# Performance work log

Hardware: AMD Instinct MI355X
Metric: run time of the kernel (lower is better)

Reference implementation:

```python
import jax, jax.numpy as jnp
import numpy as np

GAMMA = 0.96875
SCALE_BASE = 512.0


def _fixed_pos_embedding(scale):
    # scale: (L, d) where d = head_dim // 2
    L, d = scale.shape
    inv_freq = 1.0 / (10000.0 ** (jnp.arange(d, dtype=jnp.float32) / d))
    sinusoid = jnp.arange(L, dtype=jnp.float32)[:, None] * inv_freq  # (L, d)
    return jnp.sin(sinusoid), jnp.cos(sinusoid)


def _rotate_every_two(x):
    # (..., D) -> (..., D) with pairs (x0, x1) -> (-x1, x0)
    x1 = x[..., ::2]
    x2 = x[..., 1::2]
    return jnp.stack((-x2, x1), axis=-1).reshape(x.shape)


def _dup_interleave(m):
    # (L, d) -> (L, 2d), each column duplicated (matches rotary pairing)
    return jnp.repeat(m, 2, axis=-1)


def xpos(x, offset=0, downscale=False):
    # x: (B, S, D). Standard torchscale-style XPos rotary embedding.
    S, D = x.shape[-2], x.shape[-1]
    scale_vec = (jnp.arange(0, D, 2, dtype=jnp.float32) + 0.4 * D) / (1.4 * D)  # (D/2,)
    min_pos = -(S + offset) // 2
    max_pos = S + offset + min_pos
    power = jnp.arange(min_pos, max_pos, dtype=jnp.float32) / SCALE_BASE  # (S+offset,)
    scale = scale_vec ** power[:, None]  # (S+offset, D/2)
    sin, cos = _fixed_pos_embedding(scale)
    if scale.shape[0] > S:  # keep the last S positions
        scale, sin, cos = scale[-S:], sin[-S:], cos[-S:]
    if downscale:
        scale = 1.0 / scale
    sin = _dup_interleave(sin * scale)  # (S, D)
    cos = _dup_interleave(cos * scale)  # (S, D)
    return x * cos + _rotate_every_two(x) * sin


def _decay_mask(S, dtype):
    # D[n, m] = gamma^(n-m) if n >= m else 0  (lower triangular)
    m = jnp.arange(S)
    diff = m[:, None] - m  # (S, S)
    causal = diff >= 0
    exp = jnp.where(causal, diff, 0).astype(dtype)
    return jnp.where(causal, jnp.asarray(GAMMA, dtype) ** exp, jnp.zeros((), dtype))


def setup_inputs() -> dict:
    key = jax.random.key(0)
    kx, kq, kk, kv = jax.random.split(key, 4)
    B, S, H, Dh = 4, 4096, 2048, 256
    return {
        "x": jax.random.normal(kx, (B, S, H), dtype=jnp.float32),
        "w_q": jax.random.normal(kq, (H, Dh), dtype=jnp.float32),
        "w_k": jax.random.normal(kk, (H, Dh), dtype=jnp.float32),
        "w_v": jax.random.normal(kv, (H, Dh), dtype=jnp.float32),
    }


def reference(x, w_q, w_k, w_v):
    # x: (B, S, H) -> out: (B, S, Dh)
    B, S, _ = x.shape
    decay = _decay_mask(S, x.dtype)[None]  # (1, S, S)
    q = xpos(x @ w_q)                       # (B, S, Dh)
    k = xpos(x @ w_k, downscale=True)       # (B, S, Dh)
    v = x @ w_v                             # (B, S, Dh)
    ret = jnp.einsum("bsd,btd->bst", q, k) * decay  # (B, S, S)
    return jnp.einsum("bst,btd->bsd", ret, v)       # (B, S, Dh)
```

## Files before the change

kernel.cpp:

```cpp
#include <hip/hip_runtime.h>
#include <cstddef>
#include <cstdint>

#define Bn 4
#define Sn 4096
#define Hn 2048
#define Dn 256

typedef float f32x16 __attribute__((ext_vector_type(16)));
typedef short bf16x8 __attribute__((ext_vector_type(8)));

#define AS3 __attribute__((address_space(3)))
#define AS1 __attribute__((address_space(1)))

#define L2G -0.045803689613125f
#define GC 2.9526131e-4f

__device__ __forceinline__ unsigned short f2bf(float f) {
  union { float f; unsigned int u; } a; a.f = f;
  unsigned int r = a.u + 0x7fffu + ((a.u >> 16) & 1u);
  return (unsigned short)(r >> 16);
}
__device__ __forceinline__ float bf2f(unsigned int b) {
  union { unsigned int u; float f; } a; a.u = b << 16;
  return a.f;
}

__global__ __launch_bounds__(256) void xbf_kernel(const float* __restrict__ x,
                                                  unsigned short* __restrict__ xb) {
  const size_t g = (size_t)blockIdx.x * 256 + threadIdx.x;
  const float* src = x + g * 16;
  unsigned short* dst = xb + g * 16;
  uint4 o0, o1;
  {
    float4 v0 = ((const float4*)src)[0];
    float4 v1 = ((const float4*)src)[1];
    float4 v2 = ((const float4*)src)[2];
    float4 v3 = ((const float4*)src)[3];
    o0.x = f2bf(v0.x) | ((unsigned int)f2bf(v0.y) << 16);
    o0.y = f2bf(v0.z) | ((unsigned int)f2bf(v0.w) << 16);
    o0.z = f2bf(v1.x) | ((unsigned int)f2bf(v1.y) << 16);
    o0.w = f2bf(v1.z) | ((unsigned int)f2bf(v1.w) << 16);
    o1.x = f2bf(v2.x) | ((unsigned int)f2bf(v2.y) << 16);
    o1.y = f2bf(v2.z) | ((unsigned int)f2bf(v2.w) << 16);
    o1.z = f2bf(v3.x) | ((unsigned int)f2bf(v3.y) << 16);
    o1.w = f2bf(v3.z) | ((unsigned int)f2bf(v3.w) << 16);
  }
  ((uint4*)dst)[0] = o0;
  ((uint4*)dst)[1] = o1;
}

__global__ __launch_bounds__(256) void wt_build(const float* __restrict__ wq,
                                                const float* __restrict__ wk,
                                                const float* __restrict__ wv,
                                                unsigned short* __restrict__ wt) {
  __shared__ __align__(16) unsigned short T[64][72];
  const int tid = threadIdx.x;
  const int k0 = blockIdx.x * 64;
  const int n0 = blockIdx.y * 64;
  const float* w = (n0 < 256) ? wq : (n0 < 512 ? wk : wv);
  const int nc0 = n0 & 255;
#pragma unroll
  for (int it = 0; it < 2; ++it) {
    int flat = it * 256 + tid;
    int r = flat >> 3, c8 = flat & 7;
    const float* src = w + (size_t)(k0 + r) * 256 + nc0 + c8 * 8;
    float4 v0 = *(const float4*)src;
    float4 v1 = *(const float4*)(src + 4);
    T[c8 * 8 + 0][r] = f2bf(v0.x); T[c8 * 8 + 1][r] = f2bf(v0.y);
    T[c8 * 8 + 2][r] = f2bf(v0.z); T[c8 * 8 + 3][r] = f2bf(v0.w);
    T[c8 * 8 + 4][r] = f2bf(v1.x); T[c8 * 8 + 5][r] = f2bf(v1.y);
    T[c8 * 8 + 6][r] = f2bf(v1.z); T[c8 * 8 + 7][r] = f2bf(v1.w);
  }
  __syncthreads();
#pragma unroll
  for (int it = 0; it < 2; ++it) {
    int flat = it * 256 + tid;
    int nr = flat >> 3, kc8 = flat & 7;
    int n = n0 + nr;
    int kc_sw = kc8 ^ (n & 7);
    uint4 val = *(const uint4*)&T[nr][kc8 * 8];
    *(uint4*)((char*)wt + (size_t)n * 4096 + (size_t)k0 * 2 + kc_sw * 16) = val;
  }
}

__global__ __launch_bounds__(256, 3) void proj2_kernel(const unsigned short* __restrict__ xb,
                                                       const unsigned short* __restrict__ wt,
                                                       unsigned short* __restrict__ qkv) {
  __shared__ __align__(16) unsigned short As[128 * 64];
  __shared__ __align__(16) unsigned short Bs[128 * 64];
  const int tid = threadIdx.x;
  const int lane = tid & 63;
  const int wid = tid >> 6;
  const int wr = wid >> 1, wc = wid & 1;
  const int m0 = blockIdx.x * 128;
  const int n0 = blockIdx.y * 128;
  const int l31 = lane & 31, lh = lane >> 5;

  f32x16 acc[2][2];
#pragma unroll
  for (int i = 0; i < 2; ++i)
#pragma unroll
    for (int j = 0; j < 2; ++j) acc[i][j] = 0.0f;

  for (int k0 = 0; k0 < Hn; k0 += 64) {
    AS3 char* ldsa = (AS3 char*)As;
    AS3 char* ldsb = (AS3 char*)Bs;
#pragma unroll
    for (int i = 0; i < 4; ++i) {
      int ou = i * 4096 + wid * 1024;
      int o = ou + lane * 16;
      int row = o >> 7, colB = o & 127;
      const char* srcA = (const char*)xb + (size_t)(m0 + row) * 4096 + k0 * 2 + (colB ^ ((row & 7) << 4));
      __builtin_amdgcn_global_load_lds((const AS1 unsigned int*)srcA,
                                       (AS3 unsigned int*)(ldsa + ou), 16, 0, 0);
      const char* srcB = (const char*)wt + (size_t)(n0 + row) * 4096 + k0 * 2 + colB;
      __builtin_amdgcn_global_load_lds((const AS1 unsigned int*)srcB,
                                       (AS3 unsigned int*)(ldsb + ou), 16, 0, 0);
    }
    __syncthreads();
#pragma unroll
    for (int kc = 0; kc < 4; ++kc) {
      const int kb = kc * 32 + lh * 16;
      bf16x8 a[2], b[2];
#pragma unroll
      for (int i = 0; i < 2; ++i) {
        int mr = wr * 64 + i * 32 + l31;
        a[i] = *(const bf16x8*)((const char*)As + mr * 128 + (kb ^ ((mr & 7) << 4)));
        int nr = wc * 64 + i * 32 + l31;
        b[i] = *(const bf16x8*)((const char*)Bs + nr * 128 + (kb ^ ((nr & 7) << 4)));
      }
#pragma unroll
      for (int i = 0; i < 2; ++i)
#pragma unroll
        for (int j = 0; j < 2; ++j)
          acc[i][j] = __builtin_amdgcn_mfma_f32_32x32x16_bf16(a[i], b[j], acc[i][j], 0, 0, 0);
    }
    __syncthreads();
  }
  const bool khalf = (n0 >= 256 && n0 < 512);
#pragma unroll
  for (int i = 0; i < 2; ++i)
#pragma unroll
    for (int j = 0; j < 2; ++j)
#pragma unroll
      for (int reg = 0; reg < 16; ++reg) {
        int m = m0 + wr * 64 + i * 32 + (reg & 3) + 8 * (reg >> 2) + 4 * lh;
        int n = n0 + wc * 64 + j * 32 + l31;
        if (khalf) n = 256 + ((n - 256) ^ ((m & 7) << 3));
        qkv[(size_t)m * 768 + n] = f2bf(acc[i][j][reg]);
      }
}

__global__ __launch_bounds__(256, 2) void proj_kernel(const float* __restrict__ x,
                                                      const unsigned short* __restrict__ wt,
                                                      unsigned short* __restrict__ qkv) {
  __shared__ __align__(16) unsigned short As[128 * 64];
  __shared__ __align__(16) unsigned short Bs[128 * 64];
  const int tid = threadIdx.x;
  const int lane = tid & 63;
  const int wid = tid >> 6;
  const int wr = wid >> 1, wc = wid & 1;
  const int m0 = blockIdx.x * 128;
  const int n0 = blockIdx.y * 128;
  const int l31 = lane & 31, lh = lane >> 5;

  f32x16 acc[2][2];
#pragma unroll
  for (int i = 0; i < 2; ++i)
#pragma unroll
    for (int j = 0; j < 2; ++j) acc[i][j] = 0.0f;

  for (int k0 = 0; k0 < Hn; k0 += 64) {
    {
      AS3 char* ldsb = (AS3 char*)Bs;
#pragma unroll
      for (int i = 0; i < 4; ++i) {
        int ou = i * 4096 + wid * 1024;
        int o = ou + lane * 16;
        int row = o >> 7, col = o & 127;
        const char* src = (const char*)wt + (size_t)(n0 + row) * 4096 + k0 * 2 + col;
        __builtin_amdgcn_global_load_lds((const AS1 unsigned int*)src,
                                         (AS3 unsigned int*)(ldsb + ou), 16, 0, 0);
      }
    }
#pragma unroll
    for (int i = 0; i < 4; ++i) {
      int o = i * 256 + tid;
      int row = o >> 3, c8 = o & 7;
      const float* src = x + (size_t)(m0 + row) * 2048 + k0 + c8 * 8;
      float4 v0 = *(const float4*)src;
      float4 v1 = *(const float4*)(src + 4);
      uint4 val;
      val.x = f2bf(v0.x) | ((unsigned int)f2bf(v0.y) << 16);
      val.y = f2bf(v0.z) | ((unsigned int)f2bf(v0.w) << 16);
      val.z = f2bf(v1.x) | ((unsigned int)f2bf(v1.y) << 16);
      val.w = f2bf(v1.z) | ((unsigned int)f2bf(v1.w) << 16);
      *(uint4*)((char*)As + row * 128 + ((c8 * 16) ^ ((row & 7) << 4))) = val;
    }
    __syncthreads();
#pragma unroll
    for (int kc = 0; kc < 4; ++kc) {
      const int kb = kc * 32 + lh * 16;
      bf16x8 a[2], b[2];
#pragma unroll
      for (int i = 0; i < 2; ++i) {
        int mr = wr * 64 + i * 32 + l31;
        a[i] = *(const bf16x8*)((const char*)As + mr * 128 + (kb ^ ((mr & 7) << 4)));
        int nr = wc * 64 + i * 32 + l31;
        b[i] = *(const bf16x8*)((const char*)Bs + nr * 128 + (kb ^ ((nr & 7) << 4)));
      }
#pragma unroll
      for (int i = 0; i < 2; ++i)
#pragma unroll
        for (int j = 0; j < 2; ++j)
          acc[i][j] = __builtin_amdgcn_mfma_f32_32x32x16_bf16(a[i], b[j], acc[i][j], 0, 0, 0);
    }
    __syncthreads();
  }
  const bool khalf = (n0 >= 256 && n0 < 512);
#pragma unroll
  for (int i = 0; i < 2; ++i)
#pragma unroll
    for (int j = 0; j < 2; ++j)
#pragma unroll
      for (int reg = 0; reg < 16; ++reg) {
        int m = m0 + wr * 64 + i * 32 + (reg & 3) + 8 * (reg >> 2) + 4 * lh;
        int n = n0 + wc * 64 + j * 32 + l31;
        if (khalf) n = 256 + ((n - 256) ^ ((m & 7) << 3));
        qkv[(size_t)m * 768 + n] = f2bf(acc[i][j][reg]);
      }
}

__global__ __launch_bounds__(256) void xpos_kernel(unsigned short* __restrict__ qkv) {
  const int g = blockIdx.x * 256 + threadIdx.x;
  const int m = g >> 5;
  const int c = g & 31;
  const float s = (float)(m & (Sn - 1));
  unsigned short* qrow = qkv + (size_t)m * 768;
  const int csw = c ^ (m & 7);
  uint4 qv = *(uint4*)(qrow + c * 8);
  uint4 kv = *(uint4*)(qrow + 256 + csw * 8);
  unsigned int* qu = (unsigned int*)&qv;
  unsigned int* ku = (unsigned int*)&kv;
  const float pw = (s - 2048.0f) * (1.0f / 512.0f);
  const float gp = exp2f((float)(m & 255) * L2G);
#pragma unroll
  for (int p = 0; p < 4; ++p) {
    const int jp = c * 4 + p;
    const float invf = exp2f((float)jp * (-13.287712379549449f / 128.0f));
    float sn, cs;
    sincosf(s * invf, &sn, &cs);
    const float sv = (2.0f * jp + 102.4f) * (1.0f / 358.4f);
    const float scq = exp2f(pw * log2f(sv)) * gp;
    const float sci = 1.0f / scq;
    float q0 = bf2f(qu[p] & 0xffffu), q1 = bf2f(qu[p] >> 16);
    float k0 = bf2f(ku[p] & 0xffffu), k1 = bf2f(ku[p] >> 16);
    float q0r = (q0 * cs - q1 * sn) * scq;
    float q1r = (q1 * cs + q0 * sn) * scq;
    float k0r = (k0 * cs - k1 * sn) * sci;
    float k1r = (k1 * cs + k0 * sn) * sci;
    qu[p] = f2bf(q0r) | ((unsigned int)f2bf(q1r) << 16);
    ku[p] = f2bf(k0r) | ((unsigned int)f2bf(k1r) << 16);
  }
  *(uint4*)(qrow + c * 8) = qv;
  *(uint4*)(qrow + 256 + csw * 8) = kv;
}

__global__ __launch_bounds__(256) void kvt_build(const unsigned short* __restrict__ qkv,
                                                 unsigned short* __restrict__ kt,
                                                 unsigned short* __restrict__ vt) {
  __shared__ __align__(16) unsigned short Tk[64][72];
  __shared__ __align__(16) unsigned short Tv[64][72];
  const int tid = threadIdx.x;
  const int t0 = blockIdx.x * 64;
  const int d0 = blockIdx.y * 64;
  const int b = blockIdx.z;
  const size_t rowb = ((size_t)b * Sn + t0) * 1536;
#pragma unroll
  for (int it = 0; it < 2; ++it) {
    int flat = it * 256 + tid;
    int r = flat >> 3, c8 = flat & 7;
    int kc = (d0 >> 3) + c8;
    int kcs = kc ^ (r & 7);
    uint4 kvv = *(const uint4*)((const char*)qkv + rowb + (size_t)r * 1536 + 512 + kcs * 16);
    uint4 vvv = *(const uint4*)((const char*)qkv + rowb + (size_t)r * 1536 + 1024 + (size_t)(d0 + c8 * 8) * 2);
    const unsigned short* ke = (const unsigned short*)&kvv;
    const unsigned short* ve = (const unsigned short*)&vvv;
#pragma unroll
    for (int e = 0; e < 8; ++e) { Tk[c8 * 8 + e][r] = ke[e]; Tv[c8 * 8 + e][r] = ve[e]; }
  }
  __syncthreads();
#pragma unroll
  for (int it = 0; it < 2; ++it) {
    int flat = it * 256 + tid;
    int dr = flat >> 3, tc8 = flat & 7;
    *(uint4*)(kt + (size_t)(b * 256 + d0 + dr) * 4096 + t0 + tc8 * 8) = *(const uint4*)&Tk[dr][tc8 * 8];
    *(uint4*)(vt + (size_t)(b * 256 + d0 + dr) * 4096 + t0 + tc8 * 8) = *(const uint4*)&Tv[dr][tc8 * 8];
  }
}

__global__ __launch_bounds__(256) void mbuild_kernel(const unsigned short* __restrict__ kt,
                                                     const unsigned short* __restrict__ vt,
                                                     unsigned short* __restrict__ mt) {
  const int tid = threadIdx.x;
  const int lane = tid & 63;
  const int wid = tid >> 6;
  const int l31 = lane & 31, lh = lane >> 5;
  const int jc = blockIdx.x;
  const int quad = blockIdx.y;
  const int b = blockIdx.z;
  const int d2w = ((quad >> 1) * 2 + (wid >> 1)) * 64;
  const int d1w = ((quad & 1) * 2 + (wid & 1)) * 64;
  const size_t tb = (size_t)jc * 256;

  f32x16 acc[2][2];
#pragma unroll
  for (int i = 0; i < 2; ++i)
#pragma unroll
    for (int j = 0; j < 2; ++j) acc[i][j] = 0.0f;

#pragma unroll 2
  for (int dc = 0; dc < 16; ++dc) {
    const int ko = dc * 32 + lh * 16;
    bf16x8 a[2], bb[2];
#pragma unroll
    for (int i = 0; i < 2; ++i) {
      a[i]  = *(const bf16x8*)((const char*)vt + ((size_t)(b * 256 + d2w + i * 32 + l31) * 4096 + tb) * 2 + ko);
      bb[i] = *(const bf16x8*)((const char*)kt + ((size_t)(b * 256 + d1w + i * 32 + l31) * 4096 + tb) * 2 + ko);
    }
#pragma unroll
    for (int i = 0; i < 2; ++i)
#pragma unroll
      for (int j = 0; j < 2; ++j)
        acc[i][j] = __builtin_amdgcn_mfma_f32_32x32x16_bf16(a[i], bb[j], acc[i][j], 0, 0, 0);
  }
  unsigned short* dst = mt + ((size_t)(b * 16 + jc) << 16);
#pragma unroll
  for (int i = 0; i < 2; ++i)
#pragma unroll
    for (int j = 0; j < 2; ++j)
#pragma unroll
      for (int reg = 0; reg < 16; ++reg) {
        int row = d2w + i * 32 + (reg & 3) + 8 * (reg >> 2) + 4 * lh;
        int col = d1w + j * 32 + l31;
        dst[row * 256 + col] = f2bf(acc[i][j][reg]);
      }
}

__global__ __launch_bounds__(256) void scan_kernel(unsigned short* __restrict__ mt) {
  const int e0 = (blockIdx.x * 256 + threadIdx.x) * 4;
  const int b = blockIdx.y;
  unsigned short* base = mt + ((size_t)b << 20);
  float s0 = 0.f, s1 = 0.f, s2 = 0.f, s3 = 0.f;
  for (int j = 1; j < 16; ++j) {
    unsigned short* p = base + ((size_t)(j - 1) << 16) + e0;
    uint2 mv = *(const uint2*)p;
    s0 = GC * (s0 + bf2f(mv.x & 0xffffu));
    s1 = GC * (s1 + bf2f(mv.x >> 16));
    s2 = GC * (s2 + bf2f(mv.y & 0xffffu));
    s3 = GC * (s3 + bf2f(mv.y >> 16));
    uint2 w;
    w.x = f2bf(s0) | ((unsigned int)f2bf(s1) << 16);
    w.y = f2bf(s2) | ((unsigned int)f2bf(s3) << 16);
    *(uint2*)p = w;
  }
}

__global__ __launch_bounds__(256, 2) void retc_kernel(const unsigned short* __restrict__ qkv,
                                                      const unsigned short* __restrict__ vt,
                                                      const unsigned short* __restrict__ mt,
                                                      float* __restrict__ out) {
  __shared__ float cmb[2][32][256];
  const int tid = threadIdx.x;
  const int lane = tid & 63;
  const int wid = tid >> 6;
  const int tw = wid & 1, sw = wid >> 1;
  const int l31 = lane & 31, lh = lane >> 5;
  const int st = blockIdx.x;
  const int b = blockIdx.y;
  const int j = st >> 2;
  const int s0w = st * 64 + sw * 32;

  bf16x8 qf[16];
  {
    const char* qrow = (const char*)qkv + ((size_t)b * Sn + s0w + l31) * 1536;
#pragma unroll
    for (int dc = 0; dc < 16; ++dc)
      qf[dc] = *(const bf16x8*)(qrow + dc * 32 + lh * 16);
  }

  f32x16 acc[8];
#pragma unroll
  for (int i = 0; i < 8; ++i) acc[i] = 0.0f;

  if (j > 0) {
    const char* Sj = (const char*)mt + ((size_t)(b * 16 + j - 1) << 17);
#pragma unroll 2
    for (int dc = 0; dc < 16; ++dc) {
#pragma unroll
      for (int g = 0; g < 4; ++g) {
        const int ng = tw * 4 + g;
        const int d2 = ng * 32 + l31;
        bf16x8 sbf = *(const bf16x8*)(Sj + d2 * 512 + dc * 32 + lh * 16);
        acc[ng] = __builtin_amdgcn_mfma_f32_32x32x16_bf16(qf[dc], sbf, acc[ng], 0, 0, 0);
      }
    }
  }

  const int sg = s0w + l31;
  const int ksw = (l31 & 7) << 4;
  for (int tt = (st & ~3); tt <= st; ++tt) {
    const bool diag = (tt == st);
    if (diag && tw > sw) break;
    const int t0 = tt * 64 + tw * 32;
    const bool msk = diag && (tw == sw);

    f32x16 sacc = 0.0f;
    const char* krow = (const char*)qkv + ((size_t)b * Sn + t0 + l31) * 1536 + 512;
#pragma unroll 4
    for (int dc = 0; dc < 16; ++dc) {
      bf16x8 kf = *(const bf16x8*)(krow + ((dc * 32 + lh * 16) ^ ksw));
      sacc = __builtin_amdgcn_mfma_f32_32x32x16_bf16(kf, qf[dc], sacc, 0, 0, 0);
    }
    unsigned int P[8];
#pragma unroll
    for (int k = 0; k < 8; ++k) {
      const int r0 = 2 * k;
      float f0 = sacc[r0], f1 = sacc[r0 + 1];
      if (msk) {
        const int tg0 = t0 + (r0 & 3) + 8 * (r0 >> 2) + 4 * lh;
        f0 = (sg - tg0 >= 0) ? f0 : 0.0f;
        f1 = (sg - tg0 - 1 >= 0) ? f1 : 0.0f;
      }
      unsigned int pk;
      asm("v_cvt_pk_bf16_f32 %0, %1, %2" : "=v"(pk) : "v"(f0), "v"(f1));
      P[k] = pk;
    }
    asm volatile("v_permlane32_swap_b32 %0, %1" : "+v"(P[0]), "+v"(P[2]));
    asm volatile("v_permlane32_swap_b32 %0, %1" : "+v"(P[1]), "+v"(P[3]));
    asm volatile("v_permlane32_swap_b32 %0, %1" : "+v"(P[4]), "+v"(P[6]));
    asm volatile("v_permlane32_swap_b32 %0, %1" : "+v"(P[5]), "+v"(P[7]));
#pragma unroll
    for (int kc = 0; kc < 2; ++kc) {
      uint4 pw;
      pw.x = P[kc * 4 + 0]; pw.y = P[kc * 4 + 1];
      pw.z = P[kc * 4 + 2]; pw.w = P[kc * 4 + 3];
      bf16x8 pf = *(const bf16x8*)&pw;
#pragma unroll
      for (int ng = 0; ng < 8; ++ng) {
        const int d = ng * 32 + l31;
        bf16x8 vf = *(const bf16x8*)((const char*)vt +
            ((size_t)(b * 256 + d) * 4096 + t0) * 2 + kc * 32 + lh * 16);
        acc[ng] = __builtin_amdgcn_mfma_f32_32x32x16_bf16(pf, vf, acc[ng], 0, 0, 0);
      }
    }
  }

  if (tw == 1) {
#pragma unroll
    for (int ng = 0; ng < 8; ++ng)
#pragma unroll
      for (int reg = 0; reg < 16; ++reg) {
        int sl = (reg & 3) + 8 * (reg >> 2) + 4 * lh;
        cmb[sw][sl][ng * 32 + l31] = acc[ng][reg];
      }
  }
  __syncthreads();
  if (tw == 0) {
#pragma unroll
    for (int ng = 0; ng < 8; ++ng)
#pragma unroll
      for (int reg = 0; reg < 16; ++reg) {
        int sl = (reg & 3) + 8 * (reg >> 2) + 4 * lh;
        int d = ng * 32 + l31;
        out[((size_t)(b * Sn + st * 64 + sw * 32 + sl)) * 256 + d] = acc[ng][reg] + cmb[sw][sl][d];
      }
  }
}

extern "C" void kernel_launch(void* const* d_in, const int* in_sizes, int n_in,
                              void* d_out, int out_size, void* d_ws, size_t ws_size,
                              hipStream_t stream) {
  (void)in_sizes; (void)n_in; (void)out_size;
  const float* x  = (const float*)d_in[0];
  const float* wq = (const float*)d_in[1];
  const float* wk = (const float*)d_in[2];
  const float* wv = (const float*)d_in[3];
  float* out = (float*)d_out;
  char* ws = (char*)d_ws;

  unsigned short* qkv = (unsigned short*)(ws);
  unsigned short* vt  = (unsigned short*)(ws + 25165824);
  unsigned short* kt  = (unsigned short*)(ws + 33554432);
  unsigned short* mt  = (unsigned short*)(ws + 41943040);

  const size_t NEED_BIG = 95420416;
  if (ws_size >= NEED_BIG) {
    unsigned short* xb = (unsigned short*)(ws + 25165824);
    unsigned short* wt = (unsigned short*)(ws + 92274688);
    xbf_kernel<<<8192, 256, 0, stream>>>(x, xb);
    wt_build<<<dim3(32, 12), 256, 0, stream>>>(wq, wk, wv, wt);
    proj2_kernel<<<dim3(128, 6), 256, 0, stream>>>(xb, wt, qkv);
  } else {
    unsigned short* wt = (unsigned short*)(ws + 41943040);
    wt_build<<<dim3(32, 12), 256, 0, stream>>>(wq, wk, wv, wt);
    proj_kernel<<<dim3(128, 6), 256, 0, stream>>>(x, wt, qkv);
  }
  xpos_kernel<<<2048, 256, 0, stream>>>(qkv);
  kvt_build<<<dim3(64, 4, 4), 256, 0, stream>>>(qkv, kt, vt);
  mbuild_kernel<<<dim3(16, 4, 4), 256, 0, stream>>>(kt, vt, mt);
  scan_kernel<<<dim3(64, 4), 256, 0, stream>>>(mt);
  retc_kernel<<<dim3(64, 4), 256, 0, stream>>>(qkv, vt, mt, out);
}
```

Before: 192.7 us.

## Split retention output kernel over head-dim halves and 32-row tiles

```diff
diff --git a/kernel.cpp b/kernel.cpp
--- a/kernel.cpp
+++ b/kernel.cpp
@@ -371,58 +371,62 @@
                                                       const unsigned short* __restrict__ vt,
                                                       const unsigned short* __restrict__ mt,
                                                       float* __restrict__ out) {
-  __shared__ float cmb[2][32][256];
+  __shared__ float cmb[2][32][128];
   const int tid = threadIdx.x;
   const int lane = tid & 63;
-  const int wid = tid >> 6;
-  const int tw = wid & 1, sw = wid >> 1;
+  const int tw = tid >> 6;
   const int l31 = lane & 31, lh = lane >> 5;
   const int st = blockIdx.x;
-  const int b = blockIdx.y;
-  const int j = st >> 2;
-  const int s0w = st * 64 + sw * 32;
+  const int dh = blockIdx.y;
+  const int b = blockIdx.z;
+  const int j = st >> 3;
+  const int base = st & ~7;
+  const int s0 = st * 32;
+  const int d0 = dh * 128;
 
   bf16x8 qf[16];
   {
-    const char* qrow = (const char*)qkv + ((size_t)b * Sn + s0w + l31) * 1536;
+    const char* qrow = (const char*)qkv + ((size_t)b * Sn + s0 + l31) * 1536;
 #pragma unroll
     for (int dc = 0; dc < 16; ++dc)
       qf[dc] = *(const bf16x8*)(qrow + dc * 32 + lh * 16);
   }
 
-  f32x16 acc[8];
-#pragma unroll
-  for (int i = 0; i < 8; ++i) acc[i] = 0.0f;
+  f32x16 acc[4];
+#pragma unroll
+  for (int i = 0; i < 4; ++i) acc[i] = 0.0f;
 
   if (j > 0) {
     const char* Sj = (const char*)mt + ((size_t)(b * 16 + j - 1) << 17);
-#pragma unroll 2
-    for (int dc = 0; dc < 16; ++dc) {
+#pragma unroll
+    for (int dcl = 0; dcl < 4; ++dcl) {
+      const int dc = tw * 4 + dcl;
 #pragma unroll
       for (int g = 0; g < 4; ++g) {
-        const int ng = tw * 4 + g;
-        const int d2 = ng * 32 + l31;
-        bf16x8 sbf = *(const bf16x8*)(Sj + d2 * 512 + dc * 32 + lh * 16);
-        acc[ng] = __builtin_amdgcn_mfma_f32_32x32x16_bf16(qf[dc], sbf, acc[ng], 0, 0, 0);
-      }
-    }
-  }
-
-  const int sg = s0w + l31;
+        const int d2 = d0 + g * 32 + l31;
+        bf16x8 sbf = *(const bf16x8*)(Sj + (size_t)d2 * 512 + dc * 32 + lh * 16);
+        acc[g] = __builtin_amdgcn_mfma_f32_32x32x16_bf16(qf[dc], sbf, acc[g], 0, 0, 0);
+      }
+    }
+  }
+
+  const int sg = s0 + l31;
   const int ksw = (l31 & 7) << 4;
-  for (int tt = (st & ~3); tt <= st; ++tt) {
-    const bool diag = (tt == st);
-    if (diag && tw > sw) break;
-    const int t0 = tt * 64 + tw * 32;
-    const bool msk = diag && (tw == sw);
+  for (int tt = base; tt <= st; ++tt) {
+    if (((tt - base) & 3) != tw) continue;
+    const bool msk = (tt == st);
+    const int t0 = tt * 32;
 
     f32x16 sacc = 0.0f;
     const char* krow = (const char*)qkv + ((size_t)b * Sn + t0 + l31) * 1536 + 512;
-#pragma unroll 4
+    __builtin_amdgcn_s_setprio(1);
+#pragma unroll
     for (int dc = 0; dc < 16; ++dc) {
       bf16x8 kf = *(const bf16x8*)(krow + ((dc * 32 + lh * 16) ^ ksw));
       sacc = __builtin_amdgcn_mfma_f32_32x32x16_bf16(kf, qf[dc], sacc, 0, 0, 0);
     }
+    __builtin_amdgcn_s_setprio(0);
+
     unsigned int P[8];
 #pragma unroll
     for (int k = 0; k < 8; ++k) {
@@ -441,6 +445,8 @@
     asm volatile("v_permlane32_swap_b32 %0, %1" : "+v"(P[1]), "+v"(P[3]));
     asm volatile("v_permlane32_swap_b32 %0, %1" : "+v"(P[4]), "+v"(P[6]));
     asm volatile("v_permlane32_swap_b32 %0, %1" : "+v"(P[5]), "+v"(P[7]));
+
+    __builtin_amdgcn_s_setprio(1);
 #pragma unroll
     for (int kc = 0; kc < 2; ++kc) {
       uint4 pw;
@@ -448,33 +454,54 @@
       pw.z = P[kc * 4 + 2]; pw.w = P[kc * 4 + 3];
       bf16x8 pf = *(const bf16x8*)&pw;
 #pragma unroll
-      for (int ng = 0; ng < 8; ++ng) {
-        const int d = ng * 32 + l31;
+      for (int g = 0; g < 4; ++g) {
+        const int d = d0 + g * 32 + l31;
         bf16x8 vf = *(const bf16x8*)((const char*)vt +
             ((size_t)(b * 256 + d) * 4096 + t0) * 2 + kc * 32 + lh * 16);
-        acc[ng] = __builtin_amdgcn_mfma_f32_32x32x16_bf16(pf, vf, acc[ng], 0, 0, 0);
-      }
-    }
-  }
-
+        acc[g] = __builtin_amdgcn_mfma_f32_32x32x16_bf16(pf, vf, acc[g], 0, 0, 0);
+      }
+    }
+    __builtin_amdgcn_s_setprio(0);
+  }
+
+  if (tw >= 2) {
+#pragma unroll
+    for (int g = 0; g < 4; ++g)
+#pragma unroll
+      for (int reg = 0; reg < 16; ++reg) {
+        int sl = (reg & 3) + 8 * (reg >> 2) + 4 * lh;
+        cmb[tw - 2][sl][g * 32 + l31] = acc[g][reg];
+      }
+  }
+  __syncthreads();
+  if (tw < 2) {
+#pragma unroll
+    for (int g = 0; g < 4; ++g)
+#pragma unroll
+      for (int reg = 0; reg < 16; ++reg) {
+        int sl = (reg & 3) + 8 * (reg >> 2) + 4 * lh;
+        acc[g][reg] += cmb[tw][sl][g * 32 + l31];
+      }
+  }
+  __syncthreads();
   if (tw == 1) {
 #pragma unroll
-    for (int ng = 0; ng < 8; ++ng)
+    for (int g = 0; g < 4; ++g)
 #pragma unroll
       for (int reg = 0; reg < 16; ++reg) {
         int sl = (reg & 3) + 8 * (reg >> 2) + 4 * lh;
-        cmb[sw][sl][ng * 32 + l31] = acc[ng][reg];
+        cmb[0][sl][g * 32 + l31] = acc[g][reg];
       }
   }
   __syncthreads();
   if (tw == 0) {
 #pragma unroll
-    for (int ng = 0; ng < 8; ++ng)
+    for (int g = 0; g < 4; ++g)
 #pragma unroll
       for (int reg = 0; reg < 16; ++reg) {
         int sl = (reg & 3) + 8 * (reg >> 2) + 4 * lh;
-        int d = ng * 32 + l31;
-        out[((size_t)(b * Sn + st * 64 + sw * 32 + sl)) * 256 + d] = acc[ng][reg] + cmb[sw][sl][d];
+        int c = g * 32 + l31;
+        out[((size_t)(b * Sn + s0 + sl)) * 256 + d0 + c] = acc[g][reg] + cmb[0][sl][c];
       }
   }
 }
@@ -511,5 +538,5 @@
   kvt_build<<<dim3(64, 4, 4), 256, 0, stream>>>(qkv, kt, vt);
   mbuild_kernel<<<dim3(16, 4, 4), 256, 0, stream>>>(kt, vt, mt);
   scan_kernel<<<dim3(64, 4), 256, 0, stream>>>(mt);
-  retc_kernel<<<dim3(64, 4), 256, 0, stream>>>(qkv, vt, mt, out);
-}
+  retc_kernel<<<dim3(128, 2, 4), 256, 0, stream>>>(qkv, vt, mt, out);
+}
```

After: 186.0 us. -3.5%, faster.
